# Kernel optimization log

Measured on AMD Instinct MI355X. Metric: run time of the kernel, lower is better.

Reference implementation:

```python
import jax, jax.numpy as jnp
import numpy as np

TOPK = 8
N_EXPERTS = 64
ROUTE_SCALE = 1.0


def setup_inputs() -> dict:
    key = jax.random.key(0)
    k1, k2 = jax.random.split(key)
    x = jax.random.normal(k1, (16, 256, 64, 64), dtype=jnp.float32)
    gate_w = jax.random.normal(k2, (64, 256, 3, 3), dtype=jnp.float32) * 0.02  # [E, C, kh, kw]
    bias = jnp.zeros((64,), dtype=jnp.float32)  # load-balancing bias buffer
    return {"x": x, "gate_w": gate_w, "bias": bias}


def reference(x, gate_w, bias):
    # 3x3 conv, stride 1, pad 1 (SAME), no conv bias -> expert logits [B, E, H, W]
    logits = jax.lax.conv_general_dilated(
        x, gate_w, window_strides=(1, 1), padding="SAME",
        dimension_numbers=("NCHW", "OIHW", "NCHW"))
    scores = jax.nn.sigmoid(logits)                 # [B, E, H, W]
    s = jnp.moveaxis(scores, 1, -1)                 # [B, H, W, E]
    biased = s + bias                               # bias broadcast over experts
    _, idx = jax.lax.top_k(biased, TOPK)            # [B, H, W, K] (topk on biased scores)
    w = jnp.take_along_axis(s, idx, axis=-1)        # gather UNbiased scores
    w = jax.nn.softmax(w, axis=-1) * ROUTE_SCALE    # softmax over the K selected experts
    weights = jnp.moveaxis(w, -1, 1)                # [B, K, H, W] to match torch layout
    indices = jnp.moveaxis(idx, -1, 1)              # [B, K, H, W]
    counts = jnp.zeros((N_EXPERTS,), jnp.int32).at[idx.ravel()].add(1)  # bincount
    return weights, indices, counts
```

## Files before the change

### kernel.cpp

```cpp
#include <hip/hip_runtime.h>


typedef _Float16 half8 __attribute__((ext_vector_type(8)));
typedef __attribute__((ext_vector_type(4))) float f32x4;

#define LOG2E 1.44269504f

__device__ __forceinline__ unsigned short f2h_bits(float f) {
    _Float16 h = (_Float16)f;
    unsigned short b;
    __builtin_memcpy(&b, &h, 2);
    return b;
}

constexpr int WB_U4 = 8 * 9 * 4 * 64;

__global__ __launch_bounds__(256) void gate_prep(const float* __restrict__ gw,
                                                 unsigned short* __restrict__ wB,
                                                 float* __restrict__ out) {
    int g = blockIdx.x * 256 + threadIdx.x;
    if (blockIdx.x == 0 && threadIdx.x < 64) out[1048576 + threadIdx.x] = 0.f;
    if (g >= WB_U4) return;
    int lane = g & 63;
    int nt   = (g >> 6) & 3;
    int rest = g >> 8;
    int t = rest % 9, q = rest / 9;
    int e  = nt * 16 + (lane & 15);
    int c0 = q * 32 + (lane >> 4) * 8;
    unsigned short o[8];
#pragma unroll
    for (int j = 0; j < 8; ++j)
        o[j] = f2h_bits(gw[(e * 256 + c0 + j) * 9 + t]);
    uint4 pk;
    pk.x = (unsigned)o[0] | ((unsigned)o[1] << 16);
    pk.y = (unsigned)o[2] | ((unsigned)o[3] << 16);
    pk.z = (unsigned)o[4] | ((unsigned)o[5] << 16);
    pk.w = (unsigned)o[6] | ((unsigned)o[7] << 16);
    ((uint4*)wB)[g] = pk;
}

constexpr int CSTR = 40;
constexpr int SLAB = 3 * 66 * CSTR;
constexpr int SSTR = 68;

__global__ __launch_bounds__(256, 4) void gate_main(
    const float* __restrict__ x, const float* __restrict__ bias,
    const unsigned short* __restrict__ wB, float* __restrict__ out) {
    __shared__ unsigned short xs[2 * SLAB];
    __shared__ float bias_s[64];
    __shared__ int   hist[64];

    const int tid  = threadIdx.x;
    const int lane = tid & 63;
    const int rw   = tid >> 6;
    const int blk  = blockIdx.x;
    const int b    = blk & 15;
    const int r    = blk >> 4;

    if (tid < 64) { bias_s[tid] = bias[tid]; hist[tid] = 0; }

    bool tEx[4], tOk[4];
    int  tSrc[4], tDst[4];
#pragma unroll
    for (int i = 0; i < 4; ++i) {
        int T = tid + i * 256;
        tEx[i] = (T < 792);
        int chh = T / 198, s = T - chh * 198;
        int row2 = s / 66, wp = s - row2 * 66;
        int gr = r - 1 + row2, gwc = wp - 1;
        tOk[i]  = tEx[i] && (gr >= 0) && (gr < 64) && (gwc >= 0) && (gwc < 64);
        tSrc[i] = ((b * 256 + chh * 8) * 64 + gr) * 64 + gwc;
        tDst[i] = (row2 * 66 + wp) * CSTR + chh * 8;
    }

    float tb0[8], tb1[8];
    auto issue = [&](int i, int q, float* tb) {
        if (tOk[i]) {
            const float* p = x + tSrc[i] + q * 131072;
#pragma unroll
            for (int u = 0; u < 8; ++u) tb[u] = p[u * 4096];
        } else {
#pragma unroll
            for (int u = 0; u < 8; ++u) tb[u] = 0.f;
        }
    };
    auto commit = [&](int i, const float* tb, unsigned short* dst) {
        if (tEx[i]) {
            uint4 pk;
            pk.x = (unsigned)f2h_bits(tb[0]) | ((unsigned)f2h_bits(tb[1]) << 16);
            pk.y = (unsigned)f2h_bits(tb[2]) | ((unsigned)f2h_bits(tb[3]) << 16);
            pk.z = (unsigned)f2h_bits(tb[4]) | ((unsigned)f2h_bits(tb[5]) << 16);
            pk.w = (unsigned)f2h_bits(tb[6]) | ((unsigned)f2h_bits(tb[7]) << 16);
            *(uint4*)(dst + tDst[i]) = pk;
        }
    };

    const int ph = rw >> 1, eh = rw & 1;
    half8 Aa[3][2];
    uint4 Bb[3][2];
    auto prefA = [&](const unsigned short* buf, int t, int slot) {
        const int kh = t / 3, kw = t % 3;
        const unsigned short* abase =
            buf + (kh * 66 + ph * 32 + (lane & 15) + kw) * CSTR + (lane >> 4) * 8;
#pragma unroll
        for (int mt = 0; mt < 2; ++mt)
            Aa[slot][mt] = *(const half8*)(abase + mt * 16 * CSTR);
    };
    auto prefB = [&](int q, int t, int slot) {
        const uint4* bp = (const uint4*)wB + ((q * 9 + t) * 4 + eh * 2) * 64 + lane;
#pragma unroll
        for (int nt = 0; nt < 2; ++nt) Bb[slot][nt] = bp[nt * 64];
    };

    f32x4 acc[2][2];
#pragma unroll
    for (int mt = 0; mt < 2; ++mt)
#pragma unroll
        for (int nt = 0; nt < 2; ++nt) acc[mt][nt] = (f32x4){0.f, 0.f, 0.f, 0.f};

    auto mfma_tap = [&](int slot) {
#pragma unroll
        for (int nt = 0; nt < 2; ++nt) {
            half8 bfr;
            __builtin_memcpy(&bfr, &Bb[slot][nt], 16);
#pragma unroll
            for (int mt = 0; mt < 2; ++mt)
                acc[mt][nt] = __builtin_amdgcn_mfma_f32_16x16x32_f16(
                    Aa[slot][mt], bfr, acc[mt][nt], 0, 0, 0);
        }
    };

    issue(0, 0, tb0); issue(1, 0, tb1);
    commit(0, tb0, xs); commit(1, tb1, xs);
    issue(2, 0, tb0); issue(3, 0, tb1);
    commit(2, tb0, xs); commit(3, tb1, xs);
    __syncthreads();

#pragma unroll 1
    for (int q = 0; q < 8; ++q) {
        const unsigned short* cur = xs + (q & 1) * SLAB;
        unsigned short*       nxt = xs + ((q + 1) & 1) * SLAB;
        const bool st = (q < 7);
        if (st) { issue(0, q + 1, tb0); issue(1, q + 1, tb1); }
        prefA(cur, 0, 0); prefB(q, 0, 0);
        prefA(cur, 1, 1); prefB(q, 1, 1); mfma_tap(0);
        prefA(cur, 2, 2); prefB(q, 2, 2); mfma_tap(1);
        prefA(cur, 3, 0); prefB(q, 3, 0); mfma_tap(2);
        prefA(cur, 4, 1); prefB(q, 4, 1); mfma_tap(0);
        if (st) {
            commit(0, tb0, nxt); commit(1, tb1, nxt);
            issue(2, q + 1, tb0); issue(3, q + 1, tb1);
        }
        prefA(cur, 5, 2); prefB(q, 5, 2); mfma_tap(1);
        prefA(cur, 6, 0); prefB(q, 6, 0); mfma_tap(2);
        prefA(cur, 7, 1); prefB(q, 7, 1); mfma_tap(0);
        prefA(cur, 8, 2); prefB(q, 8, 2); mfma_tap(1);
        mfma_tap(2);
        if (st) { commit(2, tb0, nxt); commit(3, tb1, nxt); }
        __syncthreads();
    }

    float* scf = (float*)xs;
#pragma unroll
    for (int mt = 0; mt < 2; ++mt)
#pragma unroll
        for (int nt = 0; nt < 2; ++nt)
#pragma unroll
            for (int rr = 0; rr < 4; ++rr) {
                float v = acc[mt][nt][rr];
                float s = 1.f / (1.f + __builtin_amdgcn_exp2f(-v * LOG2E));
                int p = ph * 32 + mt * 16 + ((lane >> 4) << 2) + rr;
                int e = eh * 32 + nt * 16 + (lane & 15);
                scf[p * SSTR + e] = s;
            }
    __syncthreads();

    if (tid < 64) {
        const float* row = scf + tid * SSTR;
        float tv[8];
        int   ti[8];
#pragma unroll
        for (int k = 0; k < 8; ++k) { tv[k] = -3.0e38f; ti[k] = 0; }
#pragma unroll
        for (int j4 = 0; j4 < 16; ++j4) {
            f32x4 blkv = *(const f32x4*)(row + j4 * 4);
#pragma unroll
            for (int j = 0; j < 4; ++j) {
                int   e  = j4 * 4 + j;
                float bs = blkv[j] + bias_s[e];
                if (bs > tv[7]) {
                    tv[7] = bs; ti[7] = e;
#pragma unroll
                    for (int k = 7; k > 0; --k) {
                        float fa = tv[k - 1], fb = tv[k];
                        int   ia = ti[k - 1], ib = ti[k];
                        bool  sw = fb > fa;
                        tv[k - 1] = sw ? fb : fa; tv[k] = sw ? fa : fb;
                        ti[k - 1] = sw ? ib : ia; ti[k] = sw ? ia : ib;
                    }
                }
            }
        }
        float u[8], mx = -3.0e38f;
#pragma unroll
        for (int k = 0; k < 8; ++k) { u[k] = tv[k] - bias_s[ti[k]]; mx = fmaxf(mx, u[k]); }
        float ex[8], sum = 0.f;
#pragma unroll
        for (int k = 0; k < 8; ++k) { ex[k] = __builtin_amdgcn_exp2f((u[k] - mx) * LOG2E); sum += ex[k]; }
        float inv = 1.f / sum;

        int obase = b * 32768 + r * 64 + tid;
#pragma unroll
        for (int k = 0; k < 8; ++k) {
            out[obase + k * 4096]          = ex[k] * inv;
            out[524288 + obase + k * 4096] = (float)ti[k];
            atomicAdd(&hist[ti[k]], 1);
        }
    }
    __syncthreads();
    if (tid < 64) atomicAdd(out + 1048576 + tid, (float)hist[tid]);
}

extern "C" void kernel_launch(void* const* d_in, const int* in_sizes, int n_in,
                              void* d_out, int out_size, void* d_ws, size_t ws_size,
                              hipStream_t stream) {
    const float* x    = (const float*)d_in[0];
    const float* gw   = (const float*)d_in[1];
    const float* bias = (const float*)d_in[2];
    float* out = (float*)d_out;
    unsigned short* wB = (unsigned short*)d_ws;

    gate_prep<<<72, 256, 0, stream>>>(gw, wB, out);
    gate_main<<<1024, 256, 0, stream>>>(x, bias, wB, out);
}
```

Measured before the change: 153.3 us.

## Drop double-buffered LDS pipeline for single-buffer higher-occupancy loop, add histogram reduce kernel

Replaces the double-buffered shared-memory slab and the software-pipelined register prefetch with a single LDS buffer that is loaded and then consumed in each channel chunk. The shared output-staging area is unioned with the input slab, and launch bounds rise to 6 blocks per CU, so latency is meant to be hidden by more resident waves instead of explicit overlap. Global float atomics on the expert counts are replaced by per-block partial histograms in workspace, summed by a new single-block reduction kernel. The trade-off is an extra kernel launch, plus exposed load latency within each block and two barriers per chunk.

```diff
diff --git a/kernel.cpp b/kernel.cpp
--- a/kernel.cpp
+++ b/kernel.cpp
@@ -16,10 +16,8 @@
 constexpr int WB_U4 = 8 * 9 * 4 * 64;
 
 __global__ __launch_bounds__(256) void gate_prep(const float* __restrict__ gw,
-                                                 unsigned short* __restrict__ wB,
-                                                 float* __restrict__ out) {
+                                                 unsigned short* __restrict__ wB) {
     int g = blockIdx.x * 256 + threadIdx.x;
-    if (blockIdx.x == 0 && threadIdx.x < 64) out[1048576 + threadIdx.x] = 0.f;
     if (g >= WB_U4) return;
     int lane = g & 63;
     int nt   = (g >> 6) & 3;
@@ -39,16 +37,19 @@
     ((uint4*)wB)[g] = pk;
 }
 
-constexpr int CSTR = 40;
-constexpr int SLAB = 3 * 66 * CSTR;
-constexpr int SSTR = 68;
-
-__global__ __launch_bounds__(256, 4) void gate_main(
+constexpr int CSTR  = 40;
+constexpr int SSTR  = 68;
+constexpr int UNI_B = 64 * SSTR * 4;
+
+__global__ __launch_bounds__(256, 6) void gate_main(
     const float* __restrict__ x, const float* __restrict__ bias,
-    const unsigned short* __restrict__ wB, float* __restrict__ out) {
-    __shared__ unsigned short xs[2 * SLAB];
-    __shared__ float bias_s[64];
-    __shared__ int   hist[64];
+    const unsigned short* __restrict__ wB, float* __restrict__ out,
+    float* __restrict__ ws_hist) {
+    __shared__ unsigned char smem[UNI_B + 512];
+    unsigned short* xs     = (unsigned short*)smem;
+    float*          scf    = (float*)smem;
+    float*          bias_s = (float*)(smem + UNI_B);
+    int*            hist   = (int*)(smem + UNI_B + 256);
 
     const int tid  = threadIdx.x;
     const int lane = tid & 63;
@@ -73,94 +74,60 @@
         tDst[i] = (row2 * 66 + wp) * CSTR + chh * 8;
     }
 
-    float tb0[8], tb1[8];
-    auto issue = [&](int i, int q, float* tb) {
-        if (tOk[i]) {
-            const float* p = x + tSrc[i] + q * 131072;
-#pragma unroll
-            for (int u = 0; u < 8; ++u) tb[u] = p[u * 4096];
-        } else {
-#pragma unroll
-            for (int u = 0; u < 8; ++u) tb[u] = 0.f;
-        }
-    };
-    auto commit = [&](int i, const float* tb, unsigned short* dst) {
-        if (tEx[i]) {
-            uint4 pk;
-            pk.x = (unsigned)f2h_bits(tb[0]) | ((unsigned)f2h_bits(tb[1]) << 16);
-            pk.y = (unsigned)f2h_bits(tb[2]) | ((unsigned)f2h_bits(tb[3]) << 16);
-            pk.z = (unsigned)f2h_bits(tb[4]) | ((unsigned)f2h_bits(tb[5]) << 16);
-            pk.w = (unsigned)f2h_bits(tb[6]) | ((unsigned)f2h_bits(tb[7]) << 16);
-            *(uint4*)(dst + tDst[i]) = pk;
-        }
-    };
-
     const int ph = rw >> 1, eh = rw & 1;
-    half8 Aa[3][2];
-    uint4 Bb[3][2];
-    auto prefA = [&](const unsigned short* buf, int t, int slot) {
-        const int kh = t / 3, kw = t % 3;
-        const unsigned short* abase =
-            buf + (kh * 66 + ph * 32 + (lane & 15) + kw) * CSTR + (lane >> 4) * 8;
-#pragma unroll
-        for (int mt = 0; mt < 2; ++mt)
-            Aa[slot][mt] = *(const half8*)(abase + mt * 16 * CSTR);
-    };
-    auto prefB = [&](int q, int t, int slot) {
-        const uint4* bp = (const uint4*)wB + ((q * 9 + t) * 4 + eh * 2) * 64 + lane;
-#pragma unroll
-        for (int nt = 0; nt < 2; ++nt) Bb[slot][nt] = bp[nt * 64];
-    };
 
     f32x4 acc[2][2];
 #pragma unroll
     for (int mt = 0; mt < 2; ++mt)
 #pragma unroll
         for (int nt = 0; nt < 2; ++nt) acc[mt][nt] = (f32x4){0.f, 0.f, 0.f, 0.f};
-
-    auto mfma_tap = [&](int slot) {
-#pragma unroll
-        for (int nt = 0; nt < 2; ++nt) {
-            half8 bfr;
-            __builtin_memcpy(&bfr, &Bb[slot][nt], 16);
-#pragma unroll
-            for (int mt = 0; mt < 2; ++mt)
-                acc[mt][nt] = __builtin_amdgcn_mfma_f32_16x16x32_f16(
-                    Aa[slot][mt], bfr, acc[mt][nt], 0, 0, 0);
-        }
-    };
-
-    issue(0, 0, tb0); issue(1, 0, tb1);
-    commit(0, tb0, xs); commit(1, tb1, xs);
-    issue(2, 0, tb0); issue(3, 0, tb1);
-    commit(2, tb0, xs); commit(3, tb1, xs);
-    __syncthreads();
 
 #pragma unroll 1
     for (int q = 0; q < 8; ++q) {
-        const unsigned short* cur = xs + (q & 1) * SLAB;
-        unsigned short*       nxt = xs + ((q + 1) & 1) * SLAB;
-        const bool st = (q < 7);
-        if (st) { issue(0, q + 1, tb0); issue(1, q + 1, tb1); }
-        prefA(cur, 0, 0); prefB(q, 0, 0);
-        prefA(cur, 1, 1); prefB(q, 1, 1); mfma_tap(0);
-        prefA(cur, 2, 2); prefB(q, 2, 2); mfma_tap(1);
-        prefA(cur, 3, 0); prefB(q, 3, 0); mfma_tap(2);
-        prefA(cur, 4, 1); prefB(q, 4, 1); mfma_tap(0);
-        if (st) {
-            commit(0, tb0, nxt); commit(1, tb1, nxt);
-            issue(2, q + 1, tb0); issue(3, q + 1, tb1);
-        }
-        prefA(cur, 5, 2); prefB(q, 5, 2); mfma_tap(1);
-        prefA(cur, 6, 0); prefB(q, 6, 0); mfma_tap(2);
-        prefA(cur, 7, 1); prefB(q, 7, 1); mfma_tap(0);
-        prefA(cur, 8, 2); prefB(q, 8, 2); mfma_tap(1);
-        mfma_tap(2);
-        if (st) { commit(2, tb0, nxt); commit(3, tb1, nxt); }
         __syncthreads();
-    }
-
-    float* scf = (float*)xs;
+#pragma unroll
+        for (int i = 0; i < 4; ++i) {
+            float tb[8];
+            if (tOk[i]) {
+                const float* p = x + tSrc[i] + q * 131072;
+#pragma unroll
+                for (int u = 0; u < 8; ++u) tb[u] = p[u * 4096];
+            } else {
+#pragma unroll
+                for (int u = 0; u < 8; ++u) tb[u] = 0.f;
+            }
+            if (tEx[i]) {
+                uint4 pk;
+                pk.x = (unsigned)f2h_bits(tb[0]) | ((unsigned)f2h_bits(tb[1]) << 16);
+                pk.y = (unsigned)f2h_bits(tb[2]) | ((unsigned)f2h_bits(tb[3]) << 16);
+                pk.z = (unsigned)f2h_bits(tb[4]) | ((unsigned)f2h_bits(tb[5]) << 16);
+                pk.w = (unsigned)f2h_bits(tb[6]) | ((unsigned)f2h_bits(tb[7]) << 16);
+                *(uint4*)(xs + tDst[i]) = pk;
+            }
+        }
+        __syncthreads();
+
+#pragma unroll
+        for (int t = 0; t < 9; ++t) {
+            const int kh = t / 3, kw = t % 3;
+            const unsigned short* abase =
+                xs + (kh * 66 + ph * 32 + (lane & 15) + kw) * CSTR + (lane >> 4) * 8;
+            half8 a0 = *(const half8*)(abase);
+            half8 a1 = *(const half8*)(abase + 16 * CSTR);
+            const uint4* bp =
+                (const uint4*)wB + ((q * 9 + t) * 4 + eh * 2) * 64 + lane;
+            uint4 bu0 = bp[0], bu1 = bp[64];
+            half8 b0, b1;
+            __builtin_memcpy(&b0, &bu0, 16);
+            __builtin_memcpy(&b1, &bu1, 16);
+            acc[0][0] = __builtin_amdgcn_mfma_f32_16x16x32_f16(a0, b0, acc[0][0], 0, 0, 0);
+            acc[1][0] = __builtin_amdgcn_mfma_f32_16x16x32_f16(a1, b0, acc[1][0], 0, 0, 0);
+            acc[0][1] = __builtin_amdgcn_mfma_f32_16x16x32_f16(a0, b1, acc[0][1], 0, 0, 0);
+            acc[1][1] = __builtin_amdgcn_mfma_f32_16x16x32_f16(a1, b1, acc[1][1], 0, 0, 0);
+        }
+    }
+
+    __syncthreads();
 #pragma unroll
     for (int mt = 0; mt < 2; ++mt)
 #pragma unroll
@@ -218,7 +185,27 @@
         }
     }
     __syncthreads();
-    if (tid < 64) atomicAdd(out + 1048576 + tid, (float)hist[tid]);
+    if (tid < 64) ws_hist[blk * 64 + tid] = (float)hist[tid];
+}
+
+__global__ __launch_bounds__(256) void gate_cnt(const float* __restrict__ ws_hist,
+                                                float* __restrict__ out) {
+    __shared__ float red[256];
+    const int t = threadIdx.x;
+    const int e = t & 63, part = t >> 6;
+    float s0 = 0.f, s1 = 0.f, s2 = 0.f, s3 = 0.f, s4 = 0.f, s5 = 0.f, s6 = 0.f, s7 = 0.f;
+    const float* base = ws_hist + (size_t)part * 256 * 64 + e;
+#pragma unroll 1
+    for (int i = 0; i < 256; i += 8) {
+        s0 += base[(i + 0) * 64]; s1 += base[(i + 1) * 64];
+        s2 += base[(i + 2) * 64]; s3 += base[(i + 3) * 64];
+        s4 += base[(i + 4) * 64]; s5 += base[(i + 5) * 64];
+        s6 += base[(i + 6) * 64]; s7 += base[(i + 7) * 64];
+    }
+    red[t] = ((s0 + s1) + (s2 + s3)) + ((s4 + s5) + (s6 + s7));
+    __syncthreads();
+    if (t < 64)
+        out[1048576 + t] = (red[t] + red[t + 64]) + (red[t + 128] + red[t + 192]);
 }
 
 extern "C" void kernel_launch(void* const* d_in, const int* in_sizes, int n_in,
@@ -229,7 +216,9 @@
     const float* bias = (const float*)d_in[2];
     float* out = (float*)d_out;
     unsigned short* wB = (unsigned short*)d_ws;
-
-    gate_prep<<<72, 256, 0, stream>>>(gw, wB, out);
-    gate_main<<<1024, 256, 0, stream>>>(x, bias, wB, out);
-}
+    float* ws_hist = (float*)((char*)d_ws + 294912);
+
+    gate_prep<<<72, 256, 0, stream>>>(gw, wB);
+    gate_main<<<1024, 256, 0, stream>>>(x, bias, wB, out, ws_hist);
+    gate_cnt<<<1, 256, 0, stream>>>(ws_hist, out);
+}
```

Result: slower. 159.6 us (+4.1%).
